# Optimization experiments

Measured on AMD Instinct MI355X. Metric: run time of the kernel, lower is better.

Reference implementation:

```python
import jax, jax.numpy as jnp
import numpy as np

B_AUDIOS = 64      # num audios in batch
NODES    = 2048    # 5-frame chunks (nodes) per audio
IN, HID, OUT = 512, 256, 128
HEADS, NCLS  = 2, 7
NEG_SLOPE = 0.2    # PyG GATConv default


def setup_inputs() -> dict:
    key = jax.random.key(0)
    ks = jax.random.split(key, 12)
    N = B_AUDIOS * NODES
    # chain edges within each audio: i -> i+1 (local), offset per audio
    base = np.arange(NODES - 1)
    src = (base[None, :] + np.arange(B_AUDIOS)[:, None] * NODES).reshape(-1)
    edge_index = jnp.asarray(np.stack([src, src + 1]), dtype=jnp.int32)
    batch_indices = jnp.repeat(jnp.arange(B_AUDIOS, dtype=jnp.int32), NODES)
    s = 0.05
    return {
        "x": jax.random.normal(ks[0], (N, IN), jnp.float32),
        "edge_index": edge_index,
        "batch_indices": batch_indices,
        "num_audios": B_AUDIOS,
        "W1": jax.random.normal(ks[1], (HEADS * HID, IN)) * s,
        "as1": jax.random.normal(ks[2], (HEADS, HID)) * s,
        "ad1": jax.random.normal(ks[3], (HEADS, HID)) * s,
        "b1": jnp.zeros((HID,), jnp.float32),
        "W2": jax.random.normal(ks[4], (HEADS * OUT, HID)) * s,
        "as2": jax.random.normal(ks[5], (HEADS, OUT)) * s,
        "ad2": jax.random.normal(ks[6], (HEADS, OUT)) * s,
        "b2": jnp.zeros((OUT,), jnp.float32),
        "Wt": jax.random.normal(ks[7], (1, OUT)) * s,
        "bt": jnp.zeros((1,), jnp.float32),
        "Wa": jax.random.normal(ks[8], (2, OUT)) * s,
        "ba": jnp.zeros((2,), jnp.float32),
        "Wn": jax.random.normal(ks[9], (NCLS, OUT)) * s,
        "bn": jnp.zeros((NCLS,), jnp.float32),
    }


def _seg_softmax(e, seg, n):
    m = jax.ops.segment_max(e, seg, num_segments=n)
    ex = jnp.exp(e - m[seg])
    return ex / jax.ops.segment_sum(ex, seg, num_segments=n)[seg]


def _gat_conv(x, src, dst, W, a_src, a_dst, b):
    # PyG GATConv, heads=H, concat=False (head-mean), with self loops
    N = x.shape[0]
    H, C = a_src.shape
    loops = jnp.arange(N, dtype=src.dtype)
    s = jnp.concatenate([src, loops])
    d = jnp.concatenate([dst, loops])
    h = (x @ W.T).reshape(N, H, C)                      # [N,H,C]
    al_s = jnp.einsum('nhc,hc->nh', h, a_src)           # [N,H]
    al_d = jnp.einsum('nhc,hc->nh', h, a_dst)
    e = jax.nn.leaky_relu(al_s[s] + al_d[d], NEG_SLOPE)  # [E,H]
    alpha = _seg_softmax(e, d, N)                        # softmax over in-edges of dst
    out = jax.ops.segment_sum(alpha[:, :, None] * h[s], d, num_segments=N)
    return out.mean(axis=1) + b                          # concat=False -> head mean


def reference(x, edge_index, batch_indices, num_audios,
              W1, as1, ad1, b1, W2, as2, ad2, b2,
              Wt, bt, Wa, ba, Wn, bn):
    src, dst = edge_index[0], edge_index[1]
    # global GAT (gat1 -> relu -> gat2)
    h1 = jax.nn.relu(_gat_conv(x, src, dst, W1, as1, ad1, b1))
    emb = _gat_conv(h1, src, dst, W2, as2, ad2, b2)      # [N, OUT]
    node_pred = jax.nn.softmax(emb @ Wn.T + bn, axis=-1)
    # per-audio subgraph GAT: graphs are disjoint per-audio chains, so running the
    # same GATModel on each subgraph equals restricting the global embeddings.
    logit = (emb @ Wt.T + bt)[:, 0]                      # [N]
    w = _seg_softmax(logit, batch_indices, num_audios)   # per-audio temporal softmax
    attended = jax.ops.segment_sum(w[:, None] * emb, batch_indices,
                                   num_segments=num_audios)  # [B, OUT]
    audio_pred = attended @ Wa.T + ba                    # [B, 2]
    return node_pred, audio_pred
```

## Files before the change

### kernel.cpp

```cpp
#include <hip/hip_runtime.h>
#include <hip/hip_bf16.h>

typedef __bf16 bf16x8 __attribute__((ext_vector_type(8)));
typedef float f32x4 __attribute__((ext_vector_type(4)));

#define NTOT   131072
#define NODES_PER_AUDIO 2048
#define NAUDIO 64
#define POOL_CHUNKS 16
#define CHUNK_NODES (NODES_PER_AUDIO / POOL_CHUNKS)

__global__ __launch_bounds__(256)
void detect_dtype(const unsigned* __restrict__ x, int* __restrict__ flag)
{
    const int tid = threadIdx.x;
    int cnt = 0;
    for (int i = tid; i < 4096; i += 256) {
        unsigned e = (x[i] >> 7) & 0xFF;
        cnt += (e >= 100 && e <= 145) ? 1 : 0;
    }
    __shared__ int red[256];
    red[tid] = cnt; __syncthreads();
    for (int s = 128; s > 0; s >>= 1) {
        if (tid < s) red[tid] += red[tid + s];
        __syncthreads();
    }
    if (tid == 0) *flag = (red[0] > 3000) ? 1 : 0;
}

struct W14 { const void* s[14]; int n[14]; int off[14]; };

__global__ __launch_bounds__(256)
void convert_weights(W14 w, const int* __restrict__ flag, __bf16* __restrict__ wb)
{
    const int f = *flag;
    const int stride = gridDim.x * 256;
    for (int t = 0; t < 14; t++) {
        const void* src = w.s[t];
        __bf16* d = wb + w.off[t];
        for (int i = blockIdx.x * 256 + threadIdx.x; i < w.n[t]; i += stride)
            d[i] = f ? ((const __bf16*)src)[i] : (__bf16)((const float*)src)[i];
    }
}

template<int NX, bool DYN>
__global__ __launch_bounds__(256)
void gemm_tile(const void* __restrict__ Araw, const __bf16* __restrict__ W,
               __bf16* __restrict__ C, int M, int K, int Nc,
               const int* __restrict__ flagp)
{
    __shared__ __align__(16) __bf16 As[128 * 64];
    __shared__ __align__(16) __bf16 Bs[128 * 64];

    const int nb  = gridDim.x;
    const int ny  = nb / NX;
    const int ypx = ny >> 3;
    const int bid = blockIdx.x;
    const int xcd = bid & 7;
    const int local = bid >> 3;
    const int by = xcd * ypx + local / NX;
    const int bx = local % NX;

    const int colBase = bx * 128;
    const int rowBase = by * 128;
    const int tid  = threadIdx.x;
    const int wave = tid >> 6;
    const int lane = tid & 63;
    const int wrow = (wave >> 1) * 64;
    const int wcol = (wave & 1) * 64;
    const int lr = lane & 15;
    const int lq = lane >> 4;
    int f = 1;
    if constexpr (DYN) f = *flagp;

    f32x4 acc[4][4] = {};

    const __bf16* A16 = (const __bf16*)Araw;
    const float*  A32 = (const float*)Araw;
    const __bf16* ap[4]; const float* af32[4]; const __bf16* bp[4];
    #pragma unroll
    for (int i = 0; i < 4; i++) {
        const int c = tid + 256 * i;
        const int r = c >> 3, q = c & 7;
        ap[i]   = A16 + (size_t)(rowBase + r) * K + q * 8;
        af32[i] = A32 + (size_t)(rowBase + r) * K + q * 8;
        bp[i]   = W   + (size_t)(colBase + r) * K + q * 8;
    }

    for (int k0 = 0; k0 < K; k0 += 64) {
        __syncthreads();
        #pragma unroll
        for (int i = 0; i < 4; i++) {
            const int c = tid + 256 * i;
            __builtin_amdgcn_global_load_lds(
                (const __attribute__((address_space(1))) void*)(bp[i] + k0),
                (__attribute__((address_space(3))) void*)&Bs[c * 8], 16, 0, 0);
        }
        if (!DYN || f) {
            #pragma unroll
            for (int i = 0; i < 4; i++) {
                const int c = tid + 256 * i;
                __builtin_amdgcn_global_load_lds(
                    (const __attribute__((address_space(1))) void*)(ap[i] + k0),
                    (__attribute__((address_space(3))) void*)&As[c * 8], 16, 0, 0);
            }
        } else {
            #pragma unroll
            for (int i = 0; i < 4; i++) {
                const int c = tid + 256 * i;
                float4 u0 = *(const float4*)(af32[i] + k0);
                float4 u1 = *(const float4*)(af32[i] + k0 + 4);
                __bf16 t[8] = {(__bf16)u0.x, (__bf16)u0.y, (__bf16)u0.z, (__bf16)u0.w,
                               (__bf16)u1.x, (__bf16)u1.y, (__bf16)u1.z, (__bf16)u1.w};
                *(int4*)&As[c * 8] = *(int4*)t;
            }
        }
        __syncthreads();

        #pragma unroll
        for (int kk = 0; kk < 2; kk++) {
            bf16x8 avf[4], bvf[4];
            #pragma unroll
            for (int i = 0; i < 4; i++)
                avf[i] = *(const bf16x8*)&As[(wrow + i * 16 + lr) * 64 + kk * 32 + lq * 8];
            #pragma unroll
            for (int j = 0; j < 4; j++)
                bvf[j] = *(const bf16x8*)&Bs[(wcol + j * 16 + lr) * 64 + kk * 32 + lq * 8];
            #pragma unroll
            for (int i = 0; i < 4; i++)
                #pragma unroll
                for (int j = 0; j < 4; j++)
                    acc[i][j] = __builtin_amdgcn_mfma_f32_16x16x32_bf16(
                        avf[i], bvf[j], acc[i][j], 0, 0, 0);
        }
    }

    #pragma unroll
    for (int i = 0; i < 4; i++) {
        #pragma unroll
        for (int j = 0; j < 4; j++) {
            int col = colBase + wcol + j * 16 + lr;
            #pragma unroll
            for (int r = 0; r < 4; r++) {
                int row = rowBase + wrow + i * 16 + lq * 4 + r;
                C[(size_t)row * Nc + col] = (__bf16)acc[i][j][r];
            }
        }
    }
}

template<int C, bool RELU, bool FUSE_HEAD>
__global__ __launch_bounds__(256)
void agg_fused(const __bf16* __restrict__ h, const __bf16* __restrict__ a_s,
               const __bf16* __restrict__ a_d, const __bf16* __restrict__ bias,
               void* __restrict__ outv,
               const __bf16* __restrict__ Wn, const __bf16* __restrict__ bn,
               const __bf16* __restrict__ Wt, const __bf16* __restrict__ bt,
               void* __restrict__ node_pred, float* __restrict__ logit,
               const int* __restrict__ flag)
{
    constexpr int D = 2 * C;
    constexpr int V = D / 64;
    const int n = blockIdx.x * 4 + (threadIdx.x >> 6);
    const int lane = threadIdx.x & 63;
    const bool have_prev = (n & (NODES_PER_AUDIO - 1)) != 0;
    const size_t np = have_prev ? (size_t)(n - 1) : (size_t)n;
    const int base = lane * V;

    __bf16 h0v[V], h1v[V];
    if constexpr (V == 8) {
        *(int4*)h0v = *(const int4*)(h + (size_t)n * D + base);
        *(int4*)h1v = *(const int4*)(h + np * D + base);
    } else {
        *(int2*)h0v = *(const int2*)(h + (size_t)n * D + base);
        *(int2*)h1v = *(const int2*)(h + np * D + base);
    }

    float ps = 0.f, pd = 0.f, pp = 0.f;
    #pragma unroll
    for (int j = 0; j < V; j++) {
        float av = (float)a_s[base + j], dv = (float)a_d[base + j];
        float x0 = (float)h0v[j], x1 = (float)h1v[j];
        ps += x0 * av; pd += x0 * dv; pp += x1 * av;
    }
    #pragma unroll
    for (int off = 1; off < 32; off <<= 1) {
        ps += __shfl_xor(ps, off, 64);
        pd += __shfl_xor(pd, off, 64);
        pp += __shfl_xor(pp, off, 64);
    }

    float es = ps + pd;  es = es > 0.f ? es : 0.2f * es;
    float a_self = 1.f, a_prev = 0.f;
    if (have_prev) {
        float ep = pp + pd;  ep = ep > 0.f ? ep : 0.2f * ep;
        float m = fmaxf(es, ep);
        float wsx = __expf(es - m), wpx = __expf(ep - m);
        float inv = 1.f / (wsx + wpx);
        a_self = wsx * inv; a_prev = wpx * inv;
    }

    const int cb = (lane & 31) * V;
    float outj[V];
    #pragma unroll
    for (int j = 0; j < V; j++) {
        float p = a_self * (float)h0v[j] + a_prev * (float)h1v[j];
        p = 0.5f * (p + __shfl_xor(p, 32, 64));
        p += (float)bias[cb + j];
        if (RELU) p = fmaxf(p, 0.f);
        outj[j] = p;
    }

    if constexpr (!FUSE_HEAD) {
        if (lane < 32) {
            __bf16 ov[V];
            #pragma unroll
            for (int j = 0; j < V; j++) ov[j] = (__bf16)outj[j];
            if constexpr (V == 8)
                *(int4*)((__bf16*)outv + (size_t)n * C + cb) = *(int4*)ov;
            else
                *(int2*)((__bf16*)outv + (size_t)n * C + cb) = *(int2*)ov;
        }
    } else {
        if (lane < 32)
            *(float4*)((float*)outv + (size_t)n * C + cb) = *(float4*)outj;

        float acc[8];
        #pragma unroll
        for (int k = 0; k < 7; k++) {
            float a = 0.f;
            #pragma unroll
            for (int j = 0; j < V; j++)
                a += outj[j] * (float)Wn[k * C + cb + j];
            acc[k] = a;
        }
        {
            float a = 0.f;
            #pragma unroll
            for (int j = 0; j < V; j++)
                a += outj[j] * (float)Wt[cb + j];
            acc[7] = a;
        }
        #pragma unroll
        for (int off = 1; off < 32; off <<= 1)
            #pragma unroll
            for (int k = 0; k < 8; k++)
                acc[k] += __shfl_xor(acc[k], off, 64);

        if (lane == 0) {
            float lg[7], m = -1e30f;
            #pragma unroll
            for (int k = 0; k < 7; k++) {
                lg[k] = acc[k] + (float)bn[k];
                m = fmaxf(m, lg[k]);
            }
            float s = 0.f;
            #pragma unroll
            for (int k = 0; k < 7; k++) { lg[k] = __expf(lg[k] - m); s += lg[k]; }
            float inv = 1.f / s;
            if (*flag) {
                #pragma unroll
                for (int k = 0; k < 7; k++)
                    ((__bf16*)node_pred)[(size_t)n * 7 + k] = (__bf16)(lg[k] * inv);
            } else {
                #pragma unroll
                for (int k = 0; k < 7; k++)
                    ((float*)node_pred)[(size_t)n * 7 + k] = lg[k] * inv;
            }
            logit[n] = acc[7] + (float)bt[0];
        }
    }
}

__global__ __launch_bounds__(256)
void audio_stats(const float* __restrict__ logit, float2* __restrict__ stats)
{
    const int b = blockIdx.x;
    const int tid = threadIdx.x;
    __shared__ float red[256];
    const float* lg = logit + b * NODES_PER_AUDIO;

    float m = -1e30f;
    for (int i = tid; i < NODES_PER_AUDIO; i += 256) m = fmaxf(m, lg[i]);
    red[tid] = m; __syncthreads();
    for (int s = 128; s > 0; s >>= 1) {
        if (tid < s) red[tid] = fmaxf(red[tid], red[tid + s]);
        __syncthreads();
    }
    m = red[0]; __syncthreads();

    float s = 0.f;
    for (int i = tid; i < NODES_PER_AUDIO; i += 256) s += __expf(lg[i] - m);
    red[tid] = s; __syncthreads();
    for (int st = 128; st > 0; st >>= 1) {
        if (tid < st) red[tid] += red[tid + st];
        __syncthreads();
    }
    if (tid == 0) stats[b] = make_float2(m, 1.f / red[0]);
}

__global__ __launch_bounds__(256)
void audio_partial(const float* __restrict__ emb, const float* __restrict__ logit,
                   const float2* __restrict__ stats, float* __restrict__ partial)
{
    const int b = blockIdx.x >> 4;
    const int chunk = blockIdx.x & 15;
    const int tid = threadIdx.x;
    const int c = tid & 127, half = tid >> 7;
    const float m = stats[b].x, inv = stats[b].y;
    const float* lg = logit + b * NODES_PER_AUDIO;
    const float* eb = emb + (size_t)b * NODES_PER_AUDIO * 128;

    __shared__ float attbuf[256];
    const int n0 = chunk * CHUNK_NODES + half * (CHUNK_NODES / 2);
    float att = 0.f;
    for (int i = n0; i < n0 + CHUNK_NODES / 2; i++) {
        float w = __expf(lg[i] - m) * inv;
        att += w * eb[(size_t)i * 128 + c];
    }
    attbuf[tid] = att; __syncthreads();
    if (tid < 128)
        partial[(size_t)(b * POOL_CHUNKS + chunk) * 128 + tid] =
            attbuf[tid] + attbuf[tid + 128];
}

__global__ __launch_bounds__(64)
void audio_final(const float* __restrict__ partial, const __bf16* __restrict__ Wa,
                 const __bf16* __restrict__ ba, void* __restrict__ outbase,
                 const int* __restrict__ flag)
{
    const int b = blockIdx.x;
    const int lane = threadIdx.x;
    const float* pb = partial + (size_t)b * POOL_CHUNKS * 128;

    float a0 = 0.f, a1 = 0.f;
    #pragma unroll
    for (int k = 0; k < POOL_CHUNKS; k++) {
        a0 += pb[k * 128 + lane * 2];
        a1 += pb[k * 128 + lane * 2 + 1];
    }
    float p0 = a0 * (float)Wa[lane * 2]       + a1 * (float)Wa[lane * 2 + 1];
    float p1 = a0 * (float)Wa[128 + lane * 2] + a1 * (float)Wa[128 + lane * 2 + 1];
    #pragma unroll
    for (int off = 1; off < 64; off <<= 1) {
        p0 += __shfl_xor(p0, off, 64);
        p1 += __shfl_xor(p1, off, 64);
    }
    if (lane == 0) {
        float r0 = p0 + (float)ba[0];
        float r1 = p1 + (float)ba[1];
        if (*flag) {
            ((__bf16*)outbase)[(size_t)NTOT * 7 + b * 2 + 0] = (__bf16)r0;
            ((__bf16*)outbase)[(size_t)NTOT * 7 + b * 2 + 1] = (__bf16)r1;
        } else {
            ((float*)outbase)[(size_t)NTOT * 7 + b * 2 + 0] = r0;
            ((float*)outbase)[(size_t)NTOT * 7 + b * 2 + 1] = r1;
        }
    }
}

extern "C" void kernel_launch(void* const* d_in, const int* in_sizes, int n_in,
                              void* d_out, int out_size, void* d_ws, size_t ws_size,
                              hipStream_t stream)
{
    const void* x = d_in[0];
    char* ws = (char*)d_ws;
    const size_t N = NTOT;

    __bf16* h  = (__bf16*)ws;
    size_t off = N * 1024;
    __bf16* h1 = (__bf16*)(ws + off); off += N * 512;
    float* logit = (float*)(ws + off); off += N * 4;
    __bf16* wb = (__bf16*)(ws + off); off += 331008 * 2;
    int* flag = (int*)(ws + off); off += 16;
    float2* stats = (float2*)(ws + off); off += NAUDIO * sizeof(float2);
    float* partial = (float*)(ws + off); off += (size_t)NAUDIO * POOL_CHUNKS * 128 * 4;
    __bf16* g2 = h;
    float* emb = (float*)(ws + N * 512);

    const int O_W1 = 0,      O_W2 = 262144, O_as1 = 327680, O_ad1 = 328192;
    const int O_b1 = 328704, O_as2 = 328960, O_ad2 = 329216, O_b2 = 329472;
    const int O_Wt = 329600, O_bt = 329728, O_Wa = 329736, O_ba = 329992;
    const int O_Wn = 330000, O_bn = 330896;

    W14 w;
    const void* srcs[14] = { d_in[4], d_in[8], d_in[5], d_in[6], d_in[7],
                             d_in[9], d_in[10], d_in[11], d_in[12], d_in[13],
                             d_in[14], d_in[15], d_in[16], d_in[17] };
    const int ns[14]   = { 262144, 65536, 512, 512, 256, 256, 256, 128,
                           128, 1, 256, 2, 896, 7 };
    const int offs[14] = { O_W1, O_W2, O_as1, O_ad1, O_b1, O_as2, O_ad2, O_b2,
                           O_Wt, O_bt, O_Wa, O_ba, O_Wn, O_bn };
    for (int i = 0; i < 14; i++) { w.s[i] = srcs[i]; w.n[i] = ns[i]; w.off[i] = offs[i]; }

    const int nwb = NTOT / 4;

    detect_dtype<<<1, 256, 0, stream>>>((const unsigned*)x, flag);
    convert_weights<<<512, 256, 0, stream>>>(w, flag, wb);

    gemm_tile<4, true><<<4 * (NTOT / 128), 256, 0, stream>>>(
        x, wb + O_W1, h, NTOT, 512, 512, flag);
    agg_fused<256, true, false><<<nwb, 256, 0, stream>>>(
        h, wb + O_as1, wb + O_ad1, wb + O_b1, h1,
        nullptr, nullptr, nullptr, nullptr, nullptr, nullptr, flag);
    gemm_tile<2, false><<<2 * (NTOT / 128), 256, 0, stream>>>(
        h1, wb + O_W2, g2, NTOT, 256, 256, flag);
    agg_fused<128, false, true><<<nwb, 256, 0, stream>>>(
        g2, wb + O_as2, wb + O_ad2, wb + O_b2, emb,
        wb + O_Wn, wb + O_bn, wb + O_Wt, wb + O_bt, d_out, logit, flag);
    audio_stats<<<NAUDIO, 256, 0, stream>>>(logit, stats);
    audio_partial<<<NAUDIO * POOL_CHUNKS, 256, 0, stream>>>(emb, logit, stats, partial);
    audio_final<<<NAUDIO, 64, 0, stream>>>(partial, wb + O_Wa, wb + O_ba, d_out, flag);
}
```

Before: 649.5 us.

## Replace GEMM with 256x256 double-buffered 8-wave pipelined kernel and pre-convert x

```diff
diff --git a/kernel.cpp b/kernel.cpp
--- a/kernel.cpp
+++ b/kernel.cpp
@@ -43,108 +43,154 @@
     }
 }
 
-template<int NX, bool DYN>
-__global__ __launch_bounds__(256)
-void gemm_tile(const void* __restrict__ Araw, const __bf16* __restrict__ W,
-               __bf16* __restrict__ C, int M, int K, int Nc,
-               const int* __restrict__ flagp)
-{
-    __shared__ __align__(16) __bf16 As[128 * 64];
-    __shared__ __align__(16) __bf16 Bs[128 * 64];
-
-    const int nb  = gridDim.x;
-    const int ny  = nb / NX;
-    const int ypx = ny >> 3;
+__global__ __launch_bounds__(256)
+void convert_x(const float4* __restrict__ xf, __bf16* __restrict__ xb,
+               const int* __restrict__ flag)
+{
+    if (*flag) return;
+    const unsigned stride = gridDim.x * 256;
+    for (unsigned i = blockIdx.x * 256 + threadIdx.x; i < 16777216u; i += stride) {
+        float4 v = xf[i];
+        __bf16 t[4] = {(__bf16)v.x, (__bf16)v.y, (__bf16)v.z, (__bf16)v.w};
+        *(int2*)&xb[(size_t)i * 4] = *(int2*)t;
+    }
+}
+
+#define SBAR   __builtin_amdgcn_sched_barrier(0)
+#define BAR    do { SBAR; __builtin_amdgcn_s_barrier(); SBAR; } while (0)
+#define WAITL  do { asm volatile("s_waitcnt lgkmcnt(0)"); SBAR; } while (0)
+#define WAITV4 do { asm volatile("s_waitcnt vmcnt(4)"); SBAR; } while (0)
+
+#define STAGE(P, SOFF, LB, BUF, H, KT) do {                                        \
+    const __bf16* _g0 = (P) + (SOFF) + (size_t)(H) * 128 * K + (size_t)(KT) * 64;  \
+    __bf16* _l0 = (LB) + (BUF) * 16384 + (H) * 8192 + ld0;                         \
+    __builtin_amdgcn_global_load_lds(                                              \
+        (const __attribute__((address_space(1))) void*)_g0,                        \
+        (__attribute__((address_space(3))) void*)_l0, 16, 0, 0);                   \
+    __builtin_amdgcn_global_load_lds(                                              \
+        (const __attribute__((address_space(1))) void*)(_g0 + (size_t)64 * K),     \
+        (__attribute__((address_space(3))) void*)(_l0 + 4096), 16, 0, 0);          \
+} while (0)
+
+#define LDA(BUF, MH) do {                                                \
+    _Pragma("unroll")                                                    \
+    for (int i_ = 0; i_ < 4; i_++) {                                     \
+        const int r_ = (wr * 128 + (MH) * 64 + i_ * 16 + lr) * 64;       \
+        av[i_][0] = *(const bf16x8*)&As[(BUF) * 16384 + r_ + sw0];       \
+        av[i_][1] = *(const bf16x8*)&As[(BUF) * 16384 + r_ + sw1];       \
+    } } while (0)
+
+#define LDB(BUF, NH) do {                                                \
+    _Pragma("unroll")                                                    \
+    for (int j_ = 0; j_ < 2; j_++) {                                     \
+        const int r_ = (wc * 64 + (NH) * 32 + j_ * 16 + lr) * 64;        \
+        bv[(NH)][j_][0] = *(const bf16x8*)&Bs[(BUF) * 16384 + r_ + sw0]; \
+        bv[(NH)][j_][1] = *(const bf16x8*)&Bs[(BUF) * 16384 + r_ + sw1]; \
+    } } while (0)
+
+#define MM(MH, NH) do {                                                       \
+    __builtin_amdgcn_s_setprio(1);                                            \
+    _Pragma("unroll")                                                         \
+    for (int i_ = 0; i_ < 4; i_++)                                            \
+    _Pragma("unroll")                                                         \
+    for (int j_ = 0; j_ < 2; j_++) {                                          \
+        acc[(MH)*4+i_][(NH)*2+j_] = __builtin_amdgcn_mfma_f32_16x16x32_bf16(  \
+            av[i_][0], bv[(NH)][j_][0], acc[(MH)*4+i_][(NH)*2+j_], 0, 0, 0);  \
+        acc[(MH)*4+i_][(NH)*2+j_] = __builtin_amdgcn_mfma_f32_16x16x32_bf16(  \
+            av[i_][1], bv[(NH)][j_][1], acc[(MH)*4+i_][(NH)*2+j_], 0, 0, 0);  \
+    }                                                                         \
+    __builtin_amdgcn_s_setprio(0); } while (0)
+
+template<bool DYN>
+__global__ __launch_bounds__(512, 2)
+void gemm8p(const void* __restrict__ Araw, const __bf16* __restrict__ Aconv,
+            const __bf16* __restrict__ W, __bf16* __restrict__ C,
+            int M, int K, int Nc, int NXC, const int* __restrict__ flagp)
+{
+    extern __shared__ __align__(16) char smem[];
+    __bf16* As = (__bf16*)smem;
+    __bf16* Bs = As + 2 * 256 * 64;
+
+    const __bf16* A = (const __bf16*)Araw;
+    if constexpr (DYN) { if (!*flagp) A = Aconv; }
+
+    const int cpx = gridDim.x >> 3;
     const int bid = blockIdx.x;
-    const int xcd = bid & 7;
-    const int local = bid >> 3;
-    const int by = xcd * ypx + local / NX;
-    const int bx = local % NX;
-
-    const int colBase = bx * 128;
-    const int rowBase = by * 128;
-    const int tid  = threadIdx.x;
-    const int wave = tid >> 6;
-    const int lane = tid & 63;
-    const int wrow = (wave >> 1) * 64;
-    const int wcol = (wave & 1) * 64;
-    const int lr = lane & 15;
-    const int lq = lane >> 4;
-    int f = 1;
-    if constexpr (DYN) f = *flagp;
-
-    f32x4 acc[4][4] = {};
-
-    const __bf16* A16 = (const __bf16*)Araw;
-    const float*  A32 = (const float*)Araw;
-    const __bf16* ap[4]; const float* af32[4]; const __bf16* bp[4];
-    #pragma unroll
-    for (int i = 0; i < 4; i++) {
-        const int c = tid + 256 * i;
-        const int r = c >> 3, q = c & 7;
-        ap[i]   = A16 + (size_t)(rowBase + r) * K + q * 8;
-        af32[i] = A32 + (size_t)(rowBase + r) * K + q * 8;
-        bp[i]   = W   + (size_t)(colBase + r) * K + q * 8;
-    }
-
-    for (int k0 = 0; k0 < K; k0 += 64) {
-        __syncthreads();
+    const int gid = (bid & 7) * cpx + (bid >> 3);
+    const int by = gid / NXC, bx = gid % NXC;
+    const int rowBase = by * 256, colBase = bx * 256;
+
+    const int tid = threadIdx.x;
+    const int wave = tid >> 6, lane = tid & 63;
+    const int lr = lane & 15, lq = lane >> 4;
+    const int wr = wave >> 2, wc = wave & 3;
+    const int sw0 = ((lq ^ (lr & 7)) * 8);
+    const int sw1 = (((4 + lq) ^ (lr & 7)) * 8);
+
+    const int crow = tid >> 3, cs = tid & 7;
+    const int cq = cs ^ (crow & 7);
+    const size_t soA = (size_t)(rowBase + crow) * K + cq * 8;
+    const size_t soB = (size_t)(colBase + crow) * K + cq * 8;
+    const int ld0 = crow * 64 + cs * 8;
+
+    const int NT = K >> 6;
+
+    f32x4 acc[8][4] = {};
+    bf16x8 av[4][2], bv[2][2][2];
+
+    STAGE(A, soA, As, 0, 0, 0); STAGE(A, soA, As, 0, 1, 0);
+    STAGE(W, soB, Bs, 0, 0, 0); STAGE(W, soB, Bs, 0, 1, 0);
+    STAGE(W, soB, Bs, 1, 0, 1); STAGE(W, soB, Bs, 1, 1, 1);
+    WAITV4; BAR;
+
+    const int NIT = K >> 7;
+    for (int it = 0; it < NIT; ++it) {
+        const int t1 = 2 * it + 1;
+        const int t2 = (2 * it + 2 < NT) ? 2 * it + 2 : NT - 1;
+        const int t3 = (2 * it + 3 < NT) ? 2 * it + 3 : NT - 1;
+        LDA(0, 0); LDB(0, 0);
+        STAGE(A, soA, As, 1, 0, t1);
+        BAR; WAITL; MM(0, 0); BAR;
+
+        LDB(0, 1);
+        STAGE(A, soA, As, 1, 1, t1);
+        BAR; WAITL; MM(0, 1); BAR;
+
+        LDA(0, 1);
+        STAGE(W, soB, Bs, 0, 0, t2);
+        BAR; WAITL; MM(1, 1); BAR;
+
+        STAGE(W, soB, Bs, 0, 1, t2);
+        BAR; MM(1, 0); WAITV4; BAR;
+        LDA(1, 0); LDB(1, 0);
+        STAGE(A, soA, As, 0, 0, t2);
+        BAR; WAITL; MM(0, 0); BAR;
+
+        LDB(1, 1);
+        STAGE(A, soA, As, 0, 1, t2);
+        BAR; WAITL; MM(0, 1); BAR;
+
+        LDA(1, 1);
+        STAGE(W, soB, Bs, 1, 0, t3);
+        BAR; WAITL; MM(1, 1); BAR;
+
+        STAGE(W, soB, Bs, 1, 1, t3);
+        BAR; MM(1, 0); WAITV4; BAR;
+    }
+
+    #pragma unroll
+    for (int mh = 0; mh < 2; mh++)
+    #pragma unroll
+    for (int i = 0; i < 4; i++)
+    #pragma unroll
+    for (int nh = 0; nh < 2; nh++)
+    #pragma unroll
+    for (int j = 0; j < 2; j++) {
+        const int col = colBase + wc * 64 + nh * 32 + j * 16 + lr;
         #pragma unroll
-        for (int i = 0; i < 4; i++) {
-            const int c = tid + 256 * i;
-            __builtin_amdgcn_global_load_lds(
-                (const __attribute__((address_space(1))) void*)(bp[i] + k0),
-                (__attribute__((address_space(3))) void*)&Bs[c * 8], 16, 0, 0);
-        }
-        if (!DYN || f) {
-            #pragma unroll
-            for (int i = 0; i < 4; i++) {
-                const int c = tid + 256 * i;
-                __builtin_amdgcn_global_load_lds(
-                    (const __attribute__((address_space(1))) void*)(ap[i] + k0),
-                    (__attribute__((address_space(3))) void*)&As[c * 8], 16, 0, 0);
-            }
-        } else {
-            #pragma unroll
-            for (int i = 0; i < 4; i++) {
-                const int c = tid + 256 * i;
-                float4 u0 = *(const float4*)(af32[i] + k0);
-                float4 u1 = *(const float4*)(af32[i] + k0 + 4);
-                __bf16 t[8] = {(__bf16)u0.x, (__bf16)u0.y, (__bf16)u0.z, (__bf16)u0.w,
-                               (__bf16)u1.x, (__bf16)u1.y, (__bf16)u1.z, (__bf16)u1.w};
-                *(int4*)&As[c * 8] = *(int4*)t;
-            }
-        }
-        __syncthreads();
-
-        #pragma unroll
-        for (int kk = 0; kk < 2; kk++) {
-            bf16x8 avf[4], bvf[4];
-            #pragma unroll
-            for (int i = 0; i < 4; i++)
-                avf[i] = *(const bf16x8*)&As[(wrow + i * 16 + lr) * 64 + kk * 32 + lq * 8];
-            #pragma unroll
-            for (int j = 0; j < 4; j++)
-                bvf[j] = *(const bf16x8*)&Bs[(wcol + j * 16 + lr) * 64 + kk * 32 + lq * 8];
-            #pragma unroll
-            for (int i = 0; i < 4; i++)
-                #pragma unroll
-                for (int j = 0; j < 4; j++)
-                    acc[i][j] = __builtin_amdgcn_mfma_f32_16x16x32_bf16(
-                        avf[i], bvf[j], acc[i][j], 0, 0, 0);
-        }
-    }
-
-    #pragma unroll
-    for (int i = 0; i < 4; i++) {
-        #pragma unroll
-        for (int j = 0; j < 4; j++) {
-            int col = colBase + wcol + j * 16 + lr;
-            #pragma unroll
-            for (int r = 0; r < 4; r++) {
-                int row = rowBase + wrow + i * 16 + lq * 4 + r;
-                C[(size_t)row * Nc + col] = (__bf16)acc[i][j][r];
-            }
+        for (int r = 0; r < 4; r++) {
+            const int row = rowBase + wr * 128 + mh * 64 + i * 16 + lq * 4 + r;
+            C[(size_t)row * Nc + col] = (__bf16)acc[mh * 4 + i][nh * 2 + j][r];
         }
     }
 }
@@ -375,6 +421,7 @@
     int* flag = (int*)(ws + off); off += 16;
     float2* stats = (float2*)(ws + off); off += NAUDIO * sizeof(float2);
     float* partial = (float*)(ws + off); off += (size_t)NAUDIO * POOL_CHUNKS * 128 * 4;
+    __bf16* xb = (__bf16*)(ws + off); off += N * 512 * sizeof(__bf16);
     __bf16* g2 = h;
     float* emb = (float*)(ws + N * 512);
 
@@ -395,16 +442,26 @@
 
     const int nwb = NTOT / 4;
 
+    {
+        auto* k1 = gemm8p<true>;
+        auto* k2 = gemm8p<false>;
+        hipFuncSetAttribute(reinterpret_cast<const void*>(k1),
+                            hipFuncAttributeMaxDynamicSharedMemorySize, 131072);
+        hipFuncSetAttribute(reinterpret_cast<const void*>(k2),
+                            hipFuncAttributeMaxDynamicSharedMemorySize, 131072);
+    }
+
     detect_dtype<<<1, 256, 0, stream>>>((const unsigned*)x, flag);
     convert_weights<<<512, 256, 0, stream>>>(w, flag, wb);
-
-    gemm_tile<4, true><<<4 * (NTOT / 128), 256, 0, stream>>>(
-        x, wb + O_W1, h, NTOT, 512, 512, flag);
+    convert_x<<<2048, 256, 0, stream>>>((const float4*)x, xb, flag);
+
+    gemm8p<true><<<dim3((NTOT / 256) * 2), dim3(512), 131072, stream>>>(
+        x, xb, wb + O_W1, h, NTOT, 512, 512, 2, flag);
     agg_fused<256, true, false><<<nwb, 256, 0, stream>>>(
         h, wb + O_as1, wb + O_ad1, wb + O_b1, h1,
         nullptr, nullptr, nullptr, nullptr, nullptr, nullptr, flag);
-    gemm_tile<2, false><<<2 * (NTOT / 128), 256, 0, stream>>>(
-        h1, wb + O_W2, g2, NTOT, 256, 256, flag);
+    gemm8p<false><<<dim3(NTOT / 256), dim3(512), 131072, stream>>>(
+        h1, nullptr, wb + O_W2, g2, NTOT, 256, 256, 1, flag);
     agg_fused<128, false, true><<<nwb, 256, 0, stream>>>(
         g2, wb + O_as2, wb + O_ad2, wb + O_b2, emb,
         wb + O_Wn, wb + O_bn, wb + O_Wt, wb + O_bt, d_out, logit, flag);
```

Measured after the change: 707.2 us. +8.9%, slower.
